# Kernel optimization log

Measured on AMD Instinct MI355X. Metric: run time of the kernel, lower is better.

## Reference

```python
import jax, jax.numpy as jnp
import numpy as np

IN_CHANNELS = 256
NUM_CLUSTERS = 64


def setup_inputs() -> dict:
    key = jax.random.key(0)
    kx, kc, ks = jax.random.split(key, 3)
    x = jax.random.normal(kx, (32, IN_CHANNELS, 64, 64), dtype=jnp.float32)
    std = 1.0 / (NUM_CLUSTERS * IN_CHANNELS) ** 0.5
    clusters = jax.random.uniform(kc, (NUM_CLUSTERS, IN_CHANNELS), jnp.float32, -std, std)
    scale = jax.random.uniform(ks, (NUM_CLUSTERS,), jnp.float32, -1.0, 0.0)
    return {"x": x, "clusters": clusters, "scale": scale}


def reference(x, clusters, scale):
    # x: (B, C, H, W) -> (B, N, C)
    B, C, H, W = x.shape
    xf = x.reshape(B, C, H * W).transpose(0, 2, 1)  # (B, N, C)
    # scale * ||x - c||^2, expanded to avoid (B,N,K,C) intermediate
    x_sq = jnp.sum(xf * xf, axis=-1, keepdims=True)        # (B, N, 1)
    c_sq = jnp.sum(clusters * clusters, axis=-1)            # (K,)
    xc = jnp.einsum('bnc,kc->bnk', xf, clusters)            # (B, N, K)
    norm = scale[None, None, :] * (x_sq - 2.0 * xc + c_sq[None, None, :])
    theta = jax.nn.softmax(norm, axis=2)                    # (B, N, K)
    # sum_n theta * (x - c)  ->  (B, K, C)
    enc = jnp.einsum('bnk,bnc->bkc', theta, xf)
    theta_sum = jnp.sum(theta, axis=1)                      # (B, K)
    enc = enc - theta_sum[:, :, None] * clusters[None, :, :]
    return enc
```

## Files before the change

### kernel.cpp

```cpp
#include <hip/hip_runtime.h>

#define B_N 32
#define C_N 256
#define HW_N 4096
#define K_N 64
#define NT 64
#define CHUNKS 8
#define SUBT 8
#define NTHREADS 512
#define NBLOCKS (B_N * CHUNKS)

typedef __attribute__((ext_vector_type(8))) short short8;
typedef __attribute__((ext_vector_type(4))) float f32x4;

__device__ __forceinline__ unsigned short f2bf(float f) {
    unsigned int u = __builtin_bit_cast(unsigned int, f);
    u = (u + 0x7FFFu + ((u >> 16) & 1u)) >> 16;
    return (unsigned short)u;
}

__device__ __forceinline__ int xs_idx(int c, int n) {
    return (c * NT + n) ^ ((c & 7) << 3);
}
__device__ __forceinline__ int xts_idx(int n, int c) {
    int sw = (n & 7) ^ ((n >> 3) & 7);
    return (n * C_N + c) ^ (sw << 3);
}
__device__ __forceinline__ int tht_idx(int k, int n) {
    return (k * NT + n) ^ ((k & 7) << 3);
}

__launch_bounds__(NTHREADS, 2)
__global__ void se_main_kernel(const float* __restrict__ x,
                               const float* __restrict__ clusters,
                               const float* __restrict__ scale,
                               float* __restrict__ ws_enc,
                               float* __restrict__ ws_ts) {
    __shared__ unsigned short x_s[C_N * NT];
    __shared__ unsigned short xT_s[NT * C_N];
    __shared__ float xcT_s[K_N * (NT + 1)];
    __shared__ unsigned short thT_s[K_N * NT];
    __shared__ float xsqp_s[8 * NT];
    __shared__ float msm_s[8 * NT];
    __shared__ float mss_s[8 * NT];
    __shared__ float csq_s[K_N];
    __shared__ float scl_s[K_N];

    const int tid = threadIdx.x;
    const int w = tid >> 6;
    const int l = tid & 63;
    const int gid = blockIdx.x;
    const int b = gid >> 3;
    const int chunk = gid & 7;

    if (tid < K_N) {
        const float4* cr = (const float4*)(clusters + tid * C_N);
        float s = 0.f;
        #pragma unroll 16
        for (int i = 0; i < C_N / 4; ++i) {
            float4 v = cr[i];
            s += v.x * v.x + v.y * v.y + v.z * v.z + v.w * v.w;
        }
        csq_s[tid] = s;
        scl_s[tid] = scale[tid];
    }

    const int r16 = l & 15, g16 = l >> 4;
    const int u = l >> 3;
    const int ng = l & 7;

    const int nt1 = w & 3;
    const int ktp = (w >> 2) * 2;
    short8 cb[2][8];
    #pragma unroll
    for (int t = 0; t < 2; ++t) {
        int k = (ktp + t) * 16 + r16;
        #pragma unroll
        for (int st = 0; st < 8; ++st) {
            int c0 = st * 32 + g16 * 8;
            const float* p = clusters + k * C_N + c0;
            short8 v;
            #pragma unroll
            for (int j = 0; j < 8; ++j) v[j] = (short)f2bf(p[j]);
            cb[t][st] = v;
        }
    }

    const int ct0 = w * 2;
    f32x4 acc[4][2];
    #pragma unroll
    for (int a = 0; a < 4; ++a)
        #pragma unroll
        for (int cc = 0; cc < 2; ++cc) acc[a][cc] = (f32x4)0.f;
    float ts_reg[8];
    #pragma unroll
    for (int j = 0; j < 8; ++j) ts_reg[j] = 0.f;

    for (int s = 0; s < SUBT; ++s) {
        const int pos0 = chunk * (SUBT * NT) + s * NT;
        __syncthreads();

        float4 va[4], vb[4];
        #pragma unroll
        for (int p = 0; p < 4; ++p) {
            int c = w * 8 + u + p * 64;
            const float* gp = x + ((size_t)(b * C_N + c) * HW_N + pos0 + ng * 8);
            va[p] = *(const float4*)gp;
            vb[p] = *(const float4*)(gp + 4);
        }
        float xsq8[8];
        #pragma unroll
        for (int i = 0; i < 8; ++i) xsq8[i] = 0.f;
        #pragma unroll
        for (int p = 0; p < 4; ++p) {
            int c = w * 8 + u + p * 64;
            float v[8] = {va[p].x, va[p].y, va[p].z, va[p].w,
                          vb[p].x, vb[p].y, vb[p].z, vb[p].w};
            unsigned short ub[8];
            short8 pk;
            #pragma unroll
            for (int i = 0; i < 8; ++i) {
                xsq8[i] += v[i] * v[i];
                ub[i] = f2bf(v[i]);
                pk[i] = (short)ub[i];
            }
            *(short8*)&x_s[xs_idx(c, ng * 8)] = pk;
            #pragma unroll
            for (int i = 0; i < 8; ++i) {
                int n = ng * 8 + i;
                xT_s[xts_idx(n, c)] = ub[i];
            }
        }
        #pragma unroll
        for (int i = 0; i < 8; ++i) {
            float t = xsq8[i];
            t += __shfl_xor(t, 8, 64);
            t += __shfl_xor(t, 16, 64);
            t += __shfl_xor(t, 32, 64);
            xsq8[i] = t;
        }
        if (l < 8) {
            #pragma unroll
            for (int i = 0; i < 8; ++i) xsqp_s[w * NT + l * 8 + i] = xsq8[i];
        }
        __syncthreads();

        {
            f32x4 a0 = (f32x4)0.f, a1 = (f32x4)0.f;
            #pragma unroll
            for (int st = 0; st < 8; ++st) {
                int n = nt1 * 16 + r16;
                int c0 = st * 32 + g16 * 8;
                short8 af = *(const short8*)&xT_s[xts_idx(n, c0)];
                a0 = __builtin_amdgcn_mfma_f32_16x16x32_bf16(af, cb[0][st], a0, 0, 0, 0);
                a1 = __builtin_amdgcn_mfma_f32_16x16x32_bf16(af, cb[1][st], a1, 0, 0, 0);
            }
            #pragma unroll
            for (int rr = 0; rr < 4; ++rr) {
                int n = nt1 * 16 + g16 * 4 + rr;
                xcT_s[(ktp * 16 + r16) * (NT + 1) + n] = a0[rr];
                xcT_s[((ktp + 1) * 16 + r16) * (NT + 1) + n] = a1[rr];
            }
        }
        __syncthreads();

        float xsq = 0.f;
        #pragma unroll
        for (int ww = 0; ww < 8; ++ww) xsq += xsqp_s[ww * NT + l];
        float lg[8];
        float m8 = -1e30f;
        #pragma unroll
        for (int j = 0; j < 8; ++j) {
            int k = w * 8 + j;
            float xc = xcT_s[k * (NT + 1) + l];
            lg[j] = scl_s[k] * (xsq - 2.f * xc + csq_s[k]);
            m8 = fmaxf(m8, lg[j]);
        }
        msm_s[w * NT + l] = m8;
        __syncthreads();

        float M = msm_s[l];
        #pragma unroll
        for (int ww = 1; ww < 8; ++ww) M = fmaxf(M, msm_s[ww * NT + l]);
        float e[8], s8 = 0.f;
        #pragma unroll
        for (int j = 0; j < 8; ++j) { e[j] = __expf(lg[j] - M); s8 += e[j]; }
        mss_s[w * NT + l] = s8;
        __syncthreads();

        float S = 0.f;
        #pragma unroll
        for (int ww = 0; ww < 8; ++ww) S += mss_s[ww * NT + l];
        float rin = __fdividef(1.0f, S);
        #pragma unroll
        for (int j = 0; j < 8; ++j) {
            float th = e[j] * rin;
            thT_s[tht_idx(w * 8 + j, l)] = f2bf(th);
            float t = th;
            t += __shfl_xor(t, 1, 64);
            t += __shfl_xor(t, 2, 64);
            t += __shfl_xor(t, 4, 64);
            t += __shfl_xor(t, 8, 64);
            t += __shfl_xor(t, 16, 64);
            t += __shfl_xor(t, 32, 64);
            ts_reg[j] += t;
        }
        __syncthreads();

        #pragma unroll
        for (int st = 0; st < 2; ++st) {
            int n0 = st * 32 + g16 * 8;
            short8 av[4];
            #pragma unroll
            for (int kt = 0; kt < 4; ++kt)
                av[kt] = *(const short8*)&thT_s[tht_idx(kt * 16 + r16, n0)];
            #pragma unroll
            for (int cc = 0; cc < 2; ++cc) {
                int c = (ct0 + cc) * 16 + r16;
                short8 bv = *(const short8*)&x_s[xs_idx(c, n0)];
                #pragma unroll
                for (int kt = 0; kt < 4; ++kt)
                    acc[kt][cc] = __builtin_amdgcn_mfma_f32_16x16x32_bf16(av[kt], bv, acc[kt][cc], 0, 0, 0);
            }
        }
    }

    float* eb = ws_enc + (size_t)gid * (K_N * C_N);
    #pragma unroll
    for (int kt = 0; kt < 4; ++kt) {
        #pragma unroll
        for (int cc = 0; cc < 2; ++cc) {
            int c = (ct0 + cc) * 16 + r16;
            #pragma unroll
            for (int rr = 0; rr < 4; ++rr) {
                int k = kt * 16 + g16 * 4 + rr;
                eb[k * C_N + c] = acc[kt][cc][rr];
            }
        }
    }
    if (l == 0) {
        #pragma unroll
        for (int j = 0; j < 8; ++j) ws_ts[gid * K_N + w * 8 + j] = ts_reg[j];
    }
}

__global__ void se_reduce_kernel(const float* __restrict__ ws_enc,
                                 const float* __restrict__ ws_ts,
                                 const float* __restrict__ clusters,
                                 float* __restrict__ out) {
    int tid = blockIdx.x * 256 + threadIdx.x;
    int c4 = tid & 63;
    int k = (tid >> 6) & 63;
    int b = tid >> 12;
    float4 a = {0.f, 0.f, 0.f, 0.f};
    size_t base = (size_t)(b * CHUNKS) * (K_N * C_N) + k * C_N + c4 * 4;
    #pragma unroll
    for (int p = 0; p < CHUNKS; ++p) {
        float4 v = *(const float4*)(ws_enc + base + (size_t)p * (K_N * C_N));
        a.x += v.x; a.y += v.y; a.z += v.z; a.w += v.w;
    }
    float ts = 0.f;
    #pragma unroll
    for (int p = 0; p < CHUNKS; ++p) ts += ws_ts[(b * CHUNKS + p) * K_N + k];
    float4 cl = *(const float4*)(clusters + k * C_N + c4 * 4);
    float4 o;
    o.x = a.x - ts * cl.x;
    o.y = a.y - ts * cl.y;
    o.z = a.z - ts * cl.z;
    o.w = a.w - ts * cl.w;
    *(float4*)(out + (size_t)(b * K_N + k) * C_N + c4 * 4) = o;
}

extern "C" void kernel_launch(void* const* d_in, const int* in_sizes, int n_in,
                              void* d_out, int out_size, void* d_ws, size_t ws_size,
                              hipStream_t stream) {
    const float* x        = (const float*)d_in[0];
    const float* clusters = (const float*)d_in[1];
    const float* scale    = (const float*)d_in[2];
    float* out    = (float*)d_out;
    float* ws_enc = (float*)d_ws;
    float* ws_ts  = ws_enc + (size_t)NBLOCKS * K_N * C_N;

    se_main_kernel<<<NBLOCKS, NTHREADS, 0, stream>>>(x, clusters, scale, ws_enc, ws_ts);
    se_reduce_kernel<<<(B_N * K_N * 64) / 256, 256, 0, stream>>>(ws_enc, ws_ts, clusters, out);
}
```

Before: 244.7 us.

## Halve spatial tile, double chunks, prefetch x, merge softmax max/sum pass

Shrinks the per-iteration spatial tile from 64 to 32 positions and doubles the number of blocks (16 chunks per batch), so each block uses less shared memory and fewer registers and more blocks can be resident per CU. It also software-prefetches the next x tile into registers, fuses the softmax max and sum reductions into one barrier phase with online rescaling in exp2 form, and aliases the max/sum scratch onto the xT buffer. The cost is a larger partial-sum workspace and reduction (16 partials per batch), more loop iterations per element of work, and smaller MFMA batches per sync.

After: 347.4 us. +41.9%, slower.

```diff
diff --git a/kernel.cpp b/kernel.cpp
--- a/kernel.cpp
+++ b/kernel.cpp
@@ -4,13 +4,14 @@
 #define C_N 256
 #define HW_N 4096
 #define K_N 64
-#define NT 64
-#define CHUNKS 8
+#define NT 32
 #define SUBT 8
 #define NTHREADS 512
-#define NBLOCKS (B_N * CHUNKS)
+#define NBLOCKS 512
+#define XROW 40
 
 typedef __attribute__((ext_vector_type(8))) short short8;
+typedef __attribute__((ext_vector_type(4))) unsigned short ushort4v;
 typedef __attribute__((ext_vector_type(4))) float f32x4;
 
 __device__ __forceinline__ unsigned short f2bf(float f) {
@@ -19,71 +20,67 @@
     return (unsigned short)u;
 }
 
-__device__ __forceinline__ int xs_idx(int c, int n) {
-    return (c * NT + n) ^ ((c & 7) << 3);
-}
 __device__ __forceinline__ int xts_idx(int n, int c) {
-    int sw = (n & 7) ^ ((n >> 3) & 7);
+    int sw = (n & 7) ^ ((n >> 3) & 3);
     return (n * C_N + c) ^ (sw << 3);
 }
 __device__ __forceinline__ int tht_idx(int k, int n) {
-    return (k * NT + n) ^ ((k & 7) << 3);
-}
-
-__launch_bounds__(NTHREADS, 2)
+    int sw = (k & 3) ^ ((k >> 2) & 3);
+    return (k * NT + n) ^ (sw << 3);
+}
+
+__launch_bounds__(NTHREADS, 6)
 __global__ void se_main_kernel(const float* __restrict__ x,
                                const float* __restrict__ clusters,
                                const float* __restrict__ scale,
                                float* __restrict__ ws_enc,
                                float* __restrict__ ws_ts) {
-    __shared__ unsigned short x_s[C_N * NT];
+    __shared__ unsigned short x_s[C_N * XROW];
     __shared__ unsigned short xT_s[NT * C_N];
     __shared__ float xcT_s[K_N * (NT + 1)];
     __shared__ unsigned short thT_s[K_N * NT];
     __shared__ float xsqp_s[8 * NT];
-    __shared__ float msm_s[8 * NT];
-    __shared__ float mss_s[8 * NT];
     __shared__ float csq_s[K_N];
-    __shared__ float scl_s[K_N];
+    __shared__ float scl2_s[K_N];
+    float* msm_s = (float*)xT_s;
+    float* mss_s = ((float*)xT_s) + 16 * NT;
 
     const int tid = threadIdx.x;
     const int w = tid >> 6;
     const int l = tid & 63;
     const int gid = blockIdx.x;
-    const int b = gid >> 3;
-    const int chunk = gid & 7;
-
-    if (tid < K_N) {
-        const float4* cr = (const float4*)(clusters + tid * C_N);
-        float s = 0.f;
-        #pragma unroll 16
-        for (int i = 0; i < C_N / 4; ++i) {
-            float4 v = cr[i];
-            s += v.x * v.x + v.y * v.y + v.z * v.z + v.w * v.w;
-        }
-        csq_s[tid] = s;
-        scl_s[tid] = scale[tid];
-    }
-
+    const int b = gid >> 4;
+    const int chunk = gid & 15;
     const int r16 = l & 15, g16 = l >> 4;
     const int u = l >> 3;
     const int ng = l & 7;
-
-    const int nt1 = w & 3;
-    const int ktp = (w >> 2) * 2;
-    short8 cb[2][8];
-    #pragma unroll
-    for (int t = 0; t < 2; ++t) {
-        int k = (ktp + t) * 16 + r16;
-        #pragma unroll
-        for (int st = 0; st < 8; ++st) {
-            int c0 = st * 32 + g16 * 8;
-            const float* p = clusters + k * C_N + c0;
-            short8 v;
-            #pragma unroll
-            for (int j = 0; j < 8; ++j) v[j] = (short)f2bf(p[j]);
-            cb[t][st] = v;
-        }
+    const int n32 = l & 31;
+    const int kq = w * 2 + (l >> 5);
+
+    if (tid < K_N) {
+        const float4* cr = (const float4*)(clusters + tid * C_N);
+        float ss = 0.f;
+        #pragma unroll 8
+        for (int i = 0; i < C_N / 4; ++i) {
+            float4 v = cr[i];
+            ss += v.x * v.x + v.y * v.y + v.z * v.z + v.w * v.w;
+        }
+        csq_s[tid] = ss;
+        scl2_s[tid] = scale[tid] * 1.4426950408889634f;
+    }
+
+    const int kt = w >> 1;
+    const int nt1 = w & 1;
+    short8 cb[8];
+    #pragma unroll
+    for (int st = 0; st < 8; ++st) {
+        int k = kt * 16 + r16;
+        int c0 = st * 32 + g16 * 8;
+        const float* p = clusters + k * C_N + c0;
+        short8 v;
+        #pragma unroll
+        for (int j = 0; j < 8; ++j) v[j] = (short)f2bf(p[j]);
+        cb[st] = v;
     }
 
     const int ct0 = w * 2;
@@ -92,155 +89,136 @@
     for (int a = 0; a < 4; ++a)
         #pragma unroll
         for (int cc = 0; cc < 2; ++cc) acc[a][cc] = (f32x4)0.f;
-    float ts_reg[8];
-    #pragma unroll
-    for (int j = 0; j < 8; ++j) ts_reg[j] = 0.f;
+    float ts_reg[4] = {0.f, 0.f, 0.f, 0.f};
+
+    const size_t xbase = (size_t)b * C_N * HW_N + chunk * (SUBT * NT);
+    float4 pva[4];
+    #pragma unroll
+    for (int p = 0; p < 4; ++p)
+        pva[p] = *(const float4*)(x + xbase + (size_t)(w * 8 + u + p * 64) * HW_N + ng * 4);
 
     for (int s = 0; s < SUBT; ++s) {
-        const int pos0 = chunk * (SUBT * NT) + s * NT;
-        __syncthreads();
-
-        float4 va[4], vb[4];
+        __syncthreads();
+
+        float xsq4[4] = {0.f, 0.f, 0.f, 0.f};
         #pragma unroll
         for (int p = 0; p < 4; ++p) {
             int c = w * 8 + u + p * 64;
-            const float* gp = x + ((size_t)(b * C_N + c) * HW_N + pos0 + ng * 8);
-            va[p] = *(const float4*)gp;
-            vb[p] = *(const float4*)(gp + 4);
-        }
-        float xsq8[8];
-        #pragma unroll
-        for (int i = 0; i < 8; ++i) xsq8[i] = 0.f;
-        #pragma unroll
-        for (int p = 0; p < 4; ++p) {
-            int c = w * 8 + u + p * 64;
-            float v[8] = {va[p].x, va[p].y, va[p].z, va[p].w,
-                          vb[p].x, vb[p].y, vb[p].z, vb[p].w};
-            unsigned short ub[8];
-            short8 pk;
-            #pragma unroll
-            for (int i = 0; i < 8; ++i) {
-                xsq8[i] += v[i] * v[i];
-                ub[i] = f2bf(v[i]);
-                pk[i] = (short)ub[i];
-            }
-            *(short8*)&x_s[xs_idx(c, ng * 8)] = pk;
-            #pragma unroll
-            for (int i = 0; i < 8; ++i) {
-                int n = ng * 8 + i;
-                xT_s[xts_idx(n, c)] = ub[i];
-            }
-        }
-        #pragma unroll
-        for (int i = 0; i < 8; ++i) {
-            float t = xsq8[i];
+            float v0 = pva[p].x, v1 = pva[p].y, v2 = pva[p].z, v3 = pva[p].w;
+            xsq4[0] += v0 * v0; xsq4[1] += v1 * v1;
+            xsq4[2] += v2 * v2; xsq4[3] += v3 * v3;
+            unsigned short b0 = f2bf(v0), b1 = f2bf(v1), b2 = f2bf(v2), b3 = f2bf(v3);
+            ushort4v pk = {b0, b1, b2, b3};
+            *(ushort4v*)&x_s[c * XROW + ng * 4] = pk;
+            xT_s[xts_idx(ng * 4 + 0, c)] = b0;
+            xT_s[xts_idx(ng * 4 + 1, c)] = b1;
+            xT_s[xts_idx(ng * 4 + 2, c)] = b2;
+            xT_s[xts_idx(ng * 4 + 3, c)] = b3;
+        }
+        if (s + 1 < SUBT) {
+            #pragma unroll
+            for (int p = 0; p < 4; ++p)
+                pva[p] = *(const float4*)(x + xbase + (size_t)(w * 8 + u + p * 64) * HW_N
+                                          + (s + 1) * NT + ng * 4);
+        }
+        #pragma unroll
+        for (int i = 0; i < 4; ++i) {
+            float t = xsq4[i];
             t += __shfl_xor(t, 8, 64);
             t += __shfl_xor(t, 16, 64);
             t += __shfl_xor(t, 32, 64);
-            xsq8[i] = t;
-        }
-        if (l < 8) {
-            #pragma unroll
-            for (int i = 0; i < 8; ++i) xsqp_s[w * NT + l * 8 + i] = xsq8[i];
+            xsq4[i] = t;
+        }
+        if (u == 0) {
+            #pragma unroll
+            for (int i = 0; i < 4; ++i) xsqp_s[w * NT + ng * 4 + i] = xsq4[i];
         }
         __syncthreads();
 
         {
-            f32x4 a0 = (f32x4)0.f, a1 = (f32x4)0.f;
+            f32x4 a0 = (f32x4)0.f;
             #pragma unroll
             for (int st = 0; st < 8; ++st) {
-                int n = nt1 * 16 + r16;
-                int c0 = st * 32 + g16 * 8;
-                short8 af = *(const short8*)&xT_s[xts_idx(n, c0)];
-                a0 = __builtin_amdgcn_mfma_f32_16x16x32_bf16(af, cb[0][st], a0, 0, 0, 0);
-                a1 = __builtin_amdgcn_mfma_f32_16x16x32_bf16(af, cb[1][st], a1, 0, 0, 0);
+                short8 af = *(const short8*)&xT_s[xts_idx(nt1 * 16 + r16, st * 32 + g16 * 8)];
+                a0 = __builtin_amdgcn_mfma_f32_16x16x32_bf16(af, cb[st], a0, 0, 0, 0);
             }
             #pragma unroll
-            for (int rr = 0; rr < 4; ++rr) {
-                int n = nt1 * 16 + g16 * 4 + rr;
-                xcT_s[(ktp * 16 + r16) * (NT + 1) + n] = a0[rr];
-                xcT_s[((ktp + 1) * 16 + r16) * (NT + 1) + n] = a1[rr];
-            }
+            for (int rr = 0; rr < 4; ++rr)
+                xcT_s[(kt * 16 + r16) * (NT + 1) + nt1 * 16 + g16 * 4 + rr] = a0[rr];
         }
         __syncthreads();
 
         float xsq = 0.f;
         #pragma unroll
-        for (int ww = 0; ww < 8; ++ww) xsq += xsqp_s[ww * NT + l];
-        float lg[8];
-        float m8 = -1e30f;
-        #pragma unroll
-        for (int j = 0; j < 8; ++j) {
-            int k = w * 8 + j;
-            float xc = xcT_s[k * (NT + 1) + l];
-            lg[j] = scl_s[k] * (xsq - 2.f * xc + csq_s[k]);
+        for (int ww = 0; ww < 8; ++ww) xsq += xsqp_s[ww * NT + n32];
+        float lg[4], m8 = -1e30f;
+        #pragma unroll
+        for (int j = 0; j < 4; ++j) {
+            int k = kq * 4 + j;
+            float xc = xcT_s[k * (NT + 1) + n32];
+            lg[j] = scl2_s[k] * (xsq - 2.f * xc + csq_s[k]);
             m8 = fmaxf(m8, lg[j]);
         }
-        msm_s[w * NT + l] = m8;
-        __syncthreads();
-
-        float M = msm_s[l];
-        #pragma unroll
-        for (int ww = 1; ww < 8; ++ww) M = fmaxf(M, msm_s[ww * NT + l]);
-        float e[8], s8 = 0.f;
-        #pragma unroll
-        for (int j = 0; j < 8; ++j) { e[j] = __expf(lg[j] - M); s8 += e[j]; }
-        mss_s[w * NT + l] = s8;
-        __syncthreads();
-
+        float e4[4], s8 = 0.f;
+        #pragma unroll
+        for (int j = 0; j < 4; ++j) { e4[j] = exp2f(lg[j] - m8); s8 += e4[j]; }
+        msm_s[kq * NT + n32] = m8;
+        mss_s[kq * NT + n32] = s8;
+        __syncthreads();
+
+        float mv[16], M = -1e30f;
+        #pragma unroll
+        for (int g = 0; g < 16; ++g) {
+            mv[g] = msm_s[g * NT + n32];
+            M = fmaxf(M, mv[g]);
+        }
         float S = 0.f;
         #pragma unroll
-        for (int ww = 0; ww < 8; ++ww) S += mss_s[ww * NT + l];
-        float rin = __fdividef(1.0f, S);
-        #pragma unroll
-        for (int j = 0; j < 8; ++j) {
-            float th = e[j] * rin;
-            thT_s[tht_idx(w * 8 + j, l)] = f2bf(th);
+        for (int g = 0; g < 16; ++g) S += mss_s[g * NT + n32] * exp2f(mv[g] - M);
+        float fsc = __fdividef(exp2f(m8 - M), S);
+        #pragma unroll
+        for (int j = 0; j < 4; ++j) {
+            float th = e4[j] * fsc;
+            thT_s[tht_idx(kq * 4 + j, n32)] = f2bf(th);
             float t = th;
             t += __shfl_xor(t, 1, 64);
             t += __shfl_xor(t, 2, 64);
             t += __shfl_xor(t, 4, 64);
             t += __shfl_xor(t, 8, 64);
             t += __shfl_xor(t, 16, 64);
-            t += __shfl_xor(t, 32, 64);
             ts_reg[j] += t;
         }
         __syncthreads();
 
-        #pragma unroll
-        for (int st = 0; st < 2; ++st) {
-            int n0 = st * 32 + g16 * 8;
-            short8 av[4];
-            #pragma unroll
-            for (int kt = 0; kt < 4; ++kt)
-                av[kt] = *(const short8*)&thT_s[tht_idx(kt * 16 + r16, n0)];
-            #pragma unroll
-            for (int cc = 0; cc < 2; ++cc) {
-                int c = (ct0 + cc) * 16 + r16;
-                short8 bv = *(const short8*)&x_s[xs_idx(c, n0)];
-                #pragma unroll
-                for (int kt = 0; kt < 4; ++kt)
-                    acc[kt][cc] = __builtin_amdgcn_mfma_f32_16x16x32_bf16(av[kt], bv, acc[kt][cc], 0, 0, 0);
-            }
+        short8 av[4];
+        #pragma unroll
+        for (int k2 = 0; k2 < 4; ++k2)
+            av[k2] = *(const short8*)&thT_s[tht_idx(k2 * 16 + r16, g16 * 8)];
+        #pragma unroll
+        for (int cc = 0; cc < 2; ++cc) {
+            short8 bv = *(const short8*)&x_s[((ct0 + cc) * 16 + r16) * XROW + g16 * 8];
+            #pragma unroll
+            for (int k2 = 0; k2 < 4; ++k2)
+                acc[k2][cc] = __builtin_amdgcn_mfma_f32_16x16x32_bf16(av[k2], bv, acc[k2][cc], 0, 0, 0);
         }
     }
 
     float* eb = ws_enc + (size_t)gid * (K_N * C_N);
     #pragma unroll
-    for (int kt = 0; kt < 4; ++kt) {
+    for (int k2 = 0; k2 < 4; ++k2) {
         #pragma unroll
         for (int cc = 0; cc < 2; ++cc) {
             int c = (ct0 + cc) * 16 + r16;
             #pragma unroll
             for (int rr = 0; rr < 4; ++rr) {
-                int k = kt * 16 + g16 * 4 + rr;
-                eb[k * C_N + c] = acc[kt][cc][rr];
+                int k = k2 * 16 + g16 * 4 + rr;
+                eb[k * C_N + c] = acc[k2][cc][rr];
             }
         }
     }
-    if (l == 0) {
-        #pragma unroll
-        for (int j = 0; j < 8; ++j) ws_ts[gid * K_N + w * 8 + j] = ts_reg[j];
+    if ((l & 31) == 0) {
+        #pragma unroll
+        for (int j = 0; j < 4; ++j) ws_ts[gid * K_N + kq * 4 + j] = ts_reg[j];
     }
 }
 
@@ -253,15 +231,15 @@
     int k = (tid >> 6) & 63;
     int b = tid >> 12;
     float4 a = {0.f, 0.f, 0.f, 0.f};
-    size_t base = (size_t)(b * CHUNKS) * (K_N * C_N) + k * C_N + c4 * 4;
-    #pragma unroll
-    for (int p = 0; p < CHUNKS; ++p) {
+    size_t base = (size_t)(b * 16) * (K_N * C_N) + k * C_N + c4 * 4;
+    #pragma unroll
+    for (int p = 0; p < 16; ++p) {
         float4 v = *(const float4*)(ws_enc + base + (size_t)p * (K_N * C_N));
         a.x += v.x; a.y += v.y; a.z += v.z; a.w += v.w;
     }
     float ts = 0.f;
     #pragma unroll
-    for (int p = 0; p < CHUNKS; ++p) ts += ws_ts[(b * CHUNKS + p) * K_N + k];
+    for (int p = 0; p < 16; ++p) ts += ws_ts[(b * 16 + p) * K_N + k];
     float4 cl = *(const float4*)(clusters + k * C_N + c4 * 4);
     float4 o;
     o.x = a.x - ts * cl.x;
```
